# Optimization experiments

Measured on AMD Instinct MI355X. Metric: run time of the kernel, lower is better.

The kernel has to match this reference:

```python
import jax, jax.numpy as jnp
import numpy as np
from jax import lax

SHIFT_SIZE = 5
PAD = SHIFT_SIZE // 2


def _chunk_shifts(C):
    # torch.chunk(x, 5, dim=1): chunk size = ceil(C/5); shift for chunk i is i - PAD
    csz = -(-C // SHIFT_SIZE)
    return jnp.arange(C) // csz - PAD  # (C,) in [-PAD, PAD]


def _shift_along_h(x, shifts):
    # x: (B,C,H,W). Equivalent of pad+chunk+roll(dim=2)+cat+narrow: per-channel
    # zero-filled shift along H (no wraparound since |shift| <= PAD).
    B, C, H, W = x.shape
    xp = jnp.pad(x, ((0, 0), (0, 0), (PAD, PAD), (0, 0)))
    c_idx = jnp.arange(C)[:, None]              # (C,1)
    h_idx = jnp.arange(H)[None, :] + PAD - shifts[:, None]  # (C,H)
    return xp[:, c_idx, h_idx, :]               # (B,C,H,W)


def _shift_along_w(x, shifts):
    return jnp.swapaxes(_shift_along_h(jnp.swapaxes(x, 2, 3), shifts), 2, 3)


def setup_inputs() -> dict:
    key = jax.random.key(0)
    ks = jax.random.split(key, 7)
    B, H, W, C, hidden = 8, 128, 128, 256, 256
    x = jax.random.normal(ks[0], (B, H * W, C), dtype=jnp.float32)
    w1 = jax.random.normal(ks[1], (hidden, C), dtype=jnp.float32) * 0.02
    b1 = jnp.zeros((hidden,), dtype=jnp.float32)
    fan_out = 3 * 3 * hidden // hidden  # groups = hidden
    dw_w = jax.random.normal(ks[2], (hidden, 1, 3, 3), dtype=jnp.float32) * np.sqrt(2.0 / fan_out)
    dw_b = jnp.zeros((hidden,), dtype=jnp.float32)
    w2 = jax.random.normal(ks[3], (C, hidden), dtype=jnp.float32) * 0.02
    b2 = jnp.zeros((C,), dtype=jnp.float32)
    return {"x": x, "H": H, "W": W, "w1": w1, "b1": b1,
            "dw_w": dw_w, "dw_b": dw_b, "w2": w2, "b2": b2}


def reference(x, H, W, w1, b1, dw_w, dw_b, w2, b2):
    B, N, C = x.shape
    shifts = _chunk_shifts(C)

    # --- shift along H, then fc1 ---
    xn = jnp.reshape(jnp.swapaxes(x, 1, 2), (B, C, H, W))
    x_s = _shift_along_h(xn, shifts)
    x_s = jnp.swapaxes(x_s.reshape(B, C, H * W), 1, 2)   # (B,N,C)
    h = x_s @ w1.T + b1                                  # (B,N,hidden)

    # --- depthwise 3x3 conv ---
    Ch = h.shape[-1]
    himg = jnp.reshape(jnp.swapaxes(h, 1, 2), (B, Ch, H, W))
    himg = lax.conv_general_dilated(
        himg, dw_w, window_strides=(1, 1), padding=((1, 1), (1, 1)),
        feature_group_count=Ch,
        dimension_numbers=("NCHW", "OIHW", "NCHW")) + dw_b[None, :, None, None]
    h = jnp.swapaxes(himg.reshape(B, Ch, H * W), 1, 2)

    h = jax.nn.gelu(h, approximate=False)

    # --- shift along W, then fc2 ---
    hn = jnp.reshape(jnp.swapaxes(h, 1, 2), (B, Ch, H, W))
    h_s = _shift_along_w(hn, _chunk_shifts(Ch))
    h_s = jnp.swapaxes(h_s.reshape(B, Ch, H * W), 1, 2)  # (B,N,hidden)
    out = h_s @ w2.T + b2                                # (B,N,C)
    return out
```

## Files before the change

kernel.cpp:

```cpp
#include <hip/hip_runtime.h>
#include <hip/hip_bf16.h>
#include <math.h>

#define Hc   128
#define Wc   128
#define Cc   256
#define Nc   (Hc * Wc)
#define Bn   8
#define Mtot (Bn * Nc)
#define CSZ  52
#define SPAD 2

typedef unsigned short ushort4v __attribute__((ext_vector_type(4)));
typedef unsigned short ushort8  __attribute__((ext_vector_type(8)));
typedef __bf16         bf16x8   __attribute__((ext_vector_type(8)));
typedef float          f32x4    __attribute__((ext_vector_type(4)));

__device__ __forceinline__ float bf2f(unsigned short u) {
    return __uint_as_float(((unsigned)u) << 16);
}
__device__ __forceinline__ unsigned short f2bf(float f) {
    unsigned u = __float_as_uint(f);
    return (unsigned short)((u + 0x7fffu + ((u >> 16) & 1u)) >> 16);
}
__device__ __forceinline__ unsigned pk2bf(float a, float b) {
    unsigned ua = __float_as_uint(a) + 0x8000u;
    unsigned ub = __float_as_uint(b) + 0x8000u;
    return __builtin_amdgcn_perm(ub, ua, 0x07060302);
}
__device__ __forceinline__ void async16(const void* g, void* l) {
    __builtin_amdgcn_global_load_lds(
        (const __attribute__((address_space(1))) unsigned*)g,
        (__attribute__((address_space(3))) unsigned*)l, 16, 0, 0);
}

__global__ __launch_bounds__(256)
void wprep_kernel(const float* __restrict__ w1, const float* __restrict__ dw_w,
                  unsigned short* __restrict__ w1b, float* __restrict__ dwT)
{
    const int g = blockIdx.x * 256 + threadIdx.x;
    {
        float4 a = *(const float4*)(w1 + (size_t)g * 4);
        ushort4v o = { f2bf(a.x), f2bf(a.y), f2bf(a.z), f2bf(a.w) };
        *(ushort4v*)(w1b + (size_t)g * 4) = o;
    }
    if (g < 9 * Cc) dwT[(g % 9) * Cc + g / 9] = dw_w[g];
}

__global__ __launch_bounds__(256)
void fc1_mfma_kernel(const float* __restrict__ x, const unsigned short* __restrict__ w1b,
                     const float* __restrict__ b1, unsigned short* __restrict__ h1)
{
    __shared__ __bf16 As[128 * 32];
    __shared__ __bf16 Bs[128 * 32];
    __shared__ __align__(16) unsigned short Cs[128 * 136];

    const int tid  = threadIdx.x;
    const int lane = tid & 63;
    const int wave = tid >> 6;
    const int wm = (wave >> 1) * 64, wn = (wave & 1) * 64;
    const int bx = blockIdx.x;
    const size_t m0 = (size_t)bx * 128;
    const int j0 = blockIdx.y * 128;
    const int bb = bx >> 7, hh = bx & 127;
    const int r = tid >> 1, half = tid & 1;
    const int idx0 = tid, idx1 = tid + 256;

    f32x4 acc[4][4] = {};
    for (int k0 = 0; k0 < Cc; k0 += 32) {
        async16(w1b + (size_t)(j0 + (idx0 >> 2)) * Cc + k0 + (idx0 & 3) * 8, Bs + idx0 * 8);
        async16(w1b + (size_t)(j0 + (idx1 >> 2)) * Cc + k0 + (idx1 & 3) * 8, Bs + idx1 * 8);
        {
            const int kb = k0 + half * 16;
            unsigned p[8];
#pragma unroll
            for (int j = 0; j < 4; ++j) {
                const int c  = kb + j * 4;
                const int s  = c / CSZ - SPAD;
                const int hs = hh - s;
                float4 v = make_float4(0.f, 0.f, 0.f, 0.f);
                if (hs >= 0 && hs < Hc)
                    v = *(const float4*)(x + ((size_t)(bb * Nc + hs * Wc + r)) * Cc + c);
                p[j * 2]     = pk2bf(v.x, v.y);
                p[j * 2 + 1] = pk2bf(v.z, v.w);
            }
            uint4 q0, q1;
            q0.x = p[0]; q0.y = p[1]; q0.z = p[2]; q0.w = p[3];
            q1.x = p[4]; q1.y = p[5]; q1.z = p[6]; q1.w = p[7];
            *(uint4*)(As + r * 32 + half * 16)     = q0;
            *(uint4*)(As + r * 32 + half * 16 + 8) = q1;
        }
        __syncthreads();
        bf16x8 a[4], b[4];
        const int kq = (lane >> 4) * 8;
        const int rr = lane & 15;
#pragma unroll
        for (int i = 0; i < 4; ++i) {
            a[i] = *(const bf16x8*)(As + (wm + i * 16 + rr) * 32 + kq);
            b[i] = *(const bf16x8*)(Bs + (wn + i * 16 + rr) * 32 + kq);
        }
#pragma unroll
        for (int i = 0; i < 4; ++i)
#pragma unroll
            for (int j = 0; j < 4; ++j)
                acc[i][j] = __builtin_amdgcn_mfma_f32_16x16x32_bf16(a[i], b[j], acc[i][j], 0, 0, 0);
        __syncthreads();
    }

    const int cq = (lane >> 4) * 4;
    const int cc = lane & 15;
    float bv[4];
#pragma unroll
    for (int j = 0; j < 4; ++j) bv[j] = b1[j0 + wn + j * 16 + cc];
#pragma unroll
    for (int i = 0; i < 4; ++i)
#pragma unroll
        for (int j = 0; j < 4; ++j) {
            const int col = wn + j * 16 + cc;
#pragma unroll
            for (int rg = 0; rg < 4; ++rg)
                Cs[(wm + i * 16 + cq + rg) * 136 + col] = f2bf(acc[i][j][rg] + bv[j]);
        }
    __syncthreads();
    {
        const int row = tid >> 1, hf = tid & 1;
        const unsigned short* src = Cs + row * 136 + hf * 64;
        unsigned short* dst = h1 + (m0 + row) * Cc + j0 + hf * 64;
#pragma unroll
        for (int i = 0; i < 8; ++i)
            *(uint4*)(dst + i * 8) = *(const uint4*)(src + i * 8);
    }
}

__global__ __launch_bounds__(256)
void zero_borders_kernel(unsigned short* __restrict__ gsh)
{
    const int gid = blockIdx.x * 256 + threadIdx.x;
    const int cg  = gid & 31;
    const int rest = gid >> 5;
    const int wi = rest & 3;
    const int bh = rest >> 2;
    const int w  = (wi & 2) ? (wi + 124) : wi;
    uint4 z; z.x = z.y = z.z = z.w = 0u;
    *(uint4*)(gsh + ((size_t)bh * 128 + w) * Cc + cg * 8) = z;
}

__global__ __launch_bounds__(256)
void dwconv_gelu_scatter_kernel(const unsigned short* __restrict__ h1,
                                const float* __restrict__ dwT, const float* __restrict__ dw_b,
                                unsigned short* __restrict__ gsh)
{
    const int t   = threadIdx.x;
    const int cg  = t & 31;
    const int wq  = t >> 5;
    const int c0  = cg * 8;
    const int bh  = blockIdx.x >> 2;
    const int qtr = blockIdx.x & 3;
    const int bb  = bh >> 7, hh = bh & 127;
    const size_t rowb = (size_t)bb * Nc + (size_t)hh * Wc;
    const int wbase = qtr * 32 + wq * 4 - 1;

    float acc[4][8];
    {
        float4 a0 = *(const float4*)(dw_b + c0);
        float4 a1 = *(const float4*)(dw_b + c0 + 4);
#pragma unroll
        for (int i = 0; i < 4; ++i) {
            acc[i][0] = a0.x; acc[i][1] = a0.y; acc[i][2] = a0.z; acc[i][3] = a0.w;
            acc[i][4] = a1.x; acc[i][5] = a1.y; acc[i][6] = a1.z; acc[i][7] = a1.w;
        }
    }

#pragma unroll
    for (int dy = -1; dy <= 1; ++dy) {
        const int y = hh + dy;
        if (y < 0 || y >= Hc) continue;
        const unsigned short* rp = h1 + ((size_t)bb * Nc + (size_t)y * Wc) * Cc + c0;
        float in[6][8];
#pragma unroll
        for (int dx = 0; dx < 6; ++dx) {
            const int w = wbase + dx;
            ushort8 raw = {0, 0, 0, 0, 0, 0, 0, 0};
            if (w >= 0 && w < Wc) raw = *(const ushort8*)(rp + (size_t)w * Cc);
#pragma unroll
            for (int c = 0; c < 8; ++c) in[dx][c] = bf2f(raw[c]);
        }
        const float* wrow = dwT + (dy + 1) * 3 * Cc + c0;
        float wr[3][8];
#pragma unroll
        for (int tx = 0; tx < 3; ++tx) {
            float4 wa = *(const float4*)(wrow + tx * Cc);
            float4 wb = *(const float4*)(wrow + tx * Cc + 4);
            wr[tx][0] = wa.x; wr[tx][1] = wa.y; wr[tx][2] = wa.z; wr[tx][3] = wa.w;
            wr[tx][4] = wb.x; wr[tx][5] = wb.y; wr[tx][6] = wb.z; wr[tx][7] = wb.w;
        }
#pragma unroll
        for (int i = 0; i < 4; ++i)
#pragma unroll
            for (int tx = 0; tx < 3; ++tx)
#pragma unroll
                for (int c = 0; c < 8; ++c)
                    acc[i][c] += in[i + tx][c] * wr[tx][c];
    }

    const int s0 = c0 / CSZ - SPAD;
    const int s1 = (c0 + 4) / CSZ - SPAD;
#pragma unroll
    for (int i = 0; i < 4; ++i) {
        float g[8];
#pragma unroll
        for (int c = 0; c < 8; ++c) {
            const float v = acc[i][c];
            const float u = v * v;
            const float a = __builtin_fmaf(0.0713548162f, u, 1.5957691216f);
            const float e = __expf(v * a);
            g[c] = v * e * __builtin_amdgcn_rcpf(e + 1.0f);
        }
        uint2 lo, hi;
        lo.x = pk2bf(g[0], g[1]); lo.y = pk2bf(g[2], g[3]);
        hi.x = pk2bf(g[4], g[5]); hi.y = pk2bf(g[6], g[7]);
        const int wo = wbase + 1 + i;
        const int w0 = wo + s0, w1 = wo + s1;
        if ((unsigned)w0 < (unsigned)Wc) *(uint2*)(gsh + (rowb + w0) * Cc + c0)     = lo;
        if ((unsigned)w1 < (unsigned)Wc) *(uint2*)(gsh + (rowb + w1) * Cc + c0 + 4) = hi;
    }
}

__global__ __launch_bounds__(256)
void fc2_mfma_kernel(const unsigned short* __restrict__ A, const float* __restrict__ w2,
                     const float* __restrict__ b2, float* __restrict__ out)
{
    __shared__ __bf16 As[128 * 32];
    __shared__ __bf16 Bs[128 * 32];

    const int tid  = threadIdx.x;
    const int lane = tid & 63;
    const int wave = tid >> 6;
    const int wm = (wave >> 1) * 64, wn = (wave & 1) * 64;
    const size_t m0 = (size_t)blockIdx.x * 128;
    const int j0 = blockIdx.y * 128;

    const int idx0 = tid, idx1 = tid + 256;
    const int brow = tid >> 1, bch = (tid & 1) * 16;

    f32x4 acc[4][4] = {};
    for (int k0 = 0; k0 < Cc; k0 += 32) {
        async16(A + (m0 + (idx0 >> 2)) * Cc + k0 + (idx0 & 3) * 8, As + idx0 * 8);
        async16(A + (m0 + (idx1 >> 2)) * Cc + k0 + (idx1 & 3) * 8, As + idx1 * 8);
        {
            const float* src = w2 + (size_t)(j0 + brow) * Cc + k0 + bch;
            float4 v0 = *(const float4*)(src);
            float4 v1 = *(const float4*)(src + 4);
            float4 v2 = *(const float4*)(src + 8);
            float4 v3 = *(const float4*)(src + 12);
            uint4 p0, p1;
            p0.x = pk2bf(v0.x, v0.y); p0.y = pk2bf(v0.z, v0.w);
            p0.z = pk2bf(v1.x, v1.y); p0.w = pk2bf(v1.z, v1.w);
            p1.x = pk2bf(v2.x, v2.y); p1.y = pk2bf(v2.z, v2.w);
            p1.z = pk2bf(v3.x, v3.y); p1.w = pk2bf(v3.z, v3.w);
            *(uint4*)(Bs + brow * 32 + bch)     = p0;
            *(uint4*)(Bs + brow * 32 + bch + 8) = p1;
        }
        __syncthreads();
        bf16x8 a[4], b[4];
        const int kq = (lane >> 4) * 8;
        const int rr = lane & 15;
#pragma unroll
        for (int i = 0; i < 4; ++i) {
            a[i] = *(const bf16x8*)(As + (wm + i * 16 + rr) * 32 + kq);
            b[i] = *(const bf16x8*)(Bs + (wn + i * 16 + rr) * 32 + kq);
        }
#pragma unroll
        for (int i = 0; i < 4; ++i)
#pragma unroll
            for (int j = 0; j < 4; ++j)
                acc[i][j] = __builtin_amdgcn_mfma_f32_16x16x32_bf16(a[i], b[j], acc[i][j], 0, 0, 0);
        __syncthreads();
    }

    const int cq = (lane >> 4) * 4;
    const int cc = lane & 15;
    float bv[4];
#pragma unroll
    for (int j = 0; j < 4; ++j) bv[j] = b2[j0 + wn + j * 16 + cc];
#pragma unroll
    for (int i = 0; i < 4; ++i)
#pragma unroll
        for (int j = 0; j < 4; ++j) {
            const int col = j0 + wn + j * 16 + cc;
#pragma unroll
            for (int rg = 0; rg < 4; ++rg)
                out[(m0 + wm + i * 16 + cq + rg) * Cc + col] = acc[i][j][rg] + bv[j];
        }
}

extern "C" void kernel_launch(void* const* d_in, const int* in_sizes, int n_in,
                              void* d_out, int out_size, void* d_ws, size_t ws_size,
                              hipStream_t stream) {
    const float* x    = (const float*)d_in[0];
    const float* w1   = (const float*)d_in[3];
    const float* b1   = (const float*)d_in[4];
    const float* dw_w = (const float*)d_in[5];
    const float* dw_b = (const float*)d_in[6];
    const float* w2   = (const float*)d_in[7];
    const float* b2   = (const float*)d_in[8];
    float* out = (float*)d_out;

    unsigned short* h1  = (unsigned short*)d_ws;
    unsigned short* gsh = h1 + (size_t)Mtot * Cc;
    unsigned short* w1b = (unsigned short*)d_out;
    float*          dwT = (float*)(w1b + 65536);

    wprep_kernel<<<dim3(64), dim3(256), 0, stream>>>(w1, dw_w, w1b, dwT);
    fc1_mfma_kernel<<<dim3(Mtot / 128, 2), dim3(256), 0, stream>>>(x, w1b, b1, h1);
    zero_borders_kernel<<<dim3(512), dim3(256), 0, stream>>>(gsh);
    dwconv_gelu_scatter_kernel<<<dim3(4 * Mtot / 128), dim3(256), 0, stream>>>(h1, dwT, dw_b, gsh);
    fc2_mfma_kernel<<<dim3(Mtot / 128, 2), dim3(256), 0, stream>>>(gsh, w2, b2, out);
}
```

Baseline: 387.8 us.

## Double-buffer fc1/fc2 GEMM K-loop with padded LDS and XCD-aware block remap

Both GEMM kernels now use double-buffered LDS tiles. The next K-slice's global loads (register-staged for fp32 operands, async for bf16) are issued before the current MFMA block, so load latency overlaps compute. The register-converted operand tile is padded to a 40-element stride to reduce LDS bank conflicts, and fc1 reuses one shared buffer for the epilogue tile. The 2D grid is flattened to 1D with a block-index swizzle across 8 XCDs, plus a launch_bounds occupancy hint, at the cost of more registers for the in-flight loads.

```diff
diff --git a/kernel.cpp b/kernel.cpp
--- a/kernel.cpp
+++ b/kernel.cpp
@@ -47,64 +47,90 @@
     if (g < 9 * Cc) dwT[(g % 9) * Cc + g / 9] = dw_w[g];
 }
 
-__global__ __launch_bounds__(256)
+__global__ __launch_bounds__(256, 4)
 void fc1_mfma_kernel(const float* __restrict__ x, const unsigned short* __restrict__ w1b,
                      const float* __restrict__ b1, unsigned short* __restrict__ h1)
 {
-    __shared__ __bf16 As[128 * 32];
-    __shared__ __bf16 Bs[128 * 32];
-    __shared__ __align__(16) unsigned short Cs[128 * 136];
+    __shared__ __align__(16) unsigned char smem[36864];
+    __bf16* As = (__bf16*)smem;
+    __bf16* Bs = (__bf16*)(smem + 20480);
+    unsigned short* Cs = (unsigned short*)smem;
 
     const int tid  = threadIdx.x;
     const int lane = tid & 63;
     const int wave = tid >> 6;
     const int wm = (wave >> 1) * 64, wn = (wave & 1) * 64;
-    const int bx = blockIdx.x;
+
+    const int lid = ((blockIdx.x & 7) << 8) | (blockIdx.x >> 3);
+    const int bx  = lid >> 1;
+    const int j0  = (lid & 1) * 128;
     const size_t m0 = (size_t)bx * 128;
-    const int j0 = blockIdx.y * 128;
     const int bb = bx >> 7, hh = bx & 127;
     const int r = tid >> 1, half = tid & 1;
     const int idx0 = tid, idx1 = tid + 256;
 
+    float4 av[4];
+    auto loadA = [&](int t) {
+        const int kb = t * 32 + half * 16;
+#pragma unroll
+        for (int j = 0; j < 4; ++j) {
+            const int c  = kb + j * 4;
+            const int s  = c / CSZ - SPAD;
+            const int hs = hh - s;
+            av[j] = make_float4(0.f, 0.f, 0.f, 0.f);
+            if (hs >= 0 && hs < Hc)
+                av[j] = *(const float4*)(x + ((size_t)(bb * Nc + hs * Wc + r)) * Cc + c);
+        }
+    };
+    auto storeA = [&](int buf) {
+        uint4 q0, q1;
+        q0.x = pk2bf(av[0].x, av[0].y); q0.y = pk2bf(av[0].z, av[0].w);
+        q0.z = pk2bf(av[1].x, av[1].y); q0.w = pk2bf(av[1].z, av[1].w);
+        q1.x = pk2bf(av[2].x, av[2].y); q1.y = pk2bf(av[2].z, av[2].w);
+        q1.z = pk2bf(av[3].x, av[3].y); q1.w = pk2bf(av[3].z, av[3].w);
+        __bf16* dst = As + buf * (128 * 40) + r * 40 + half * 16;
+        *(uint4*)dst       = q0;
+        *(uint4*)(dst + 8) = q1;
+    };
+    auto stageB = [&](int buf, int t) {
+        const int k0 = t * 32;
+        __bf16* bdst = Bs + buf * (128 * 32);
+        async16(w1b + (size_t)(j0 + (idx0 >> 2)) * Cc + k0 + (idx0 & 3) * 8, bdst + idx0 * 8);
+        async16(w1b + (size_t)(j0 + (idx1 >> 2)) * Cc + k0 + (idx1 & 3) * 8, bdst + idx1 * 8);
+    };
+
     f32x4 acc[4][4] = {};
-    for (int k0 = 0; k0 < Cc; k0 += 32) {
-        async16(w1b + (size_t)(j0 + (idx0 >> 2)) * Cc + k0 + (idx0 & 3) * 8, Bs + idx0 * 8);
-        async16(w1b + (size_t)(j0 + (idx1 >> 2)) * Cc + k0 + (idx1 & 3) * 8, Bs + idx1 * 8);
-        {
-            const int kb = k0 + half * 16;
-            unsigned p[8];
-#pragma unroll
-            for (int j = 0; j < 4; ++j) {
-                const int c  = kb + j * 4;
-                const int s  = c / CSZ - SPAD;
-                const int hs = hh - s;
-                float4 v = make_float4(0.f, 0.f, 0.f, 0.f);
-                if (hs >= 0 && hs < Hc)
-                    v = *(const float4*)(x + ((size_t)(bb * Nc + hs * Wc + r)) * Cc + c);
-                p[j * 2]     = pk2bf(v.x, v.y);
-                p[j * 2 + 1] = pk2bf(v.z, v.w);
-            }
-            uint4 q0, q1;
-            q0.x = p[0]; q0.y = p[1]; q0.z = p[2]; q0.w = p[3];
-            q1.x = p[4]; q1.y = p[5]; q1.z = p[6]; q1.w = p[7];
-            *(uint4*)(As + r * 32 + half * 16)     = q0;
-            *(uint4*)(As + r * 32 + half * 16 + 8) = q1;
-        }
-        __syncthreads();
+
+    loadA(0);
+    stageB(0, 0);
+    storeA(0);
+    __syncthreads();
+
+    const int kq = (lane >> 4) * 8;
+    const int rr = lane & 15;
+    int cur = 0;
+    for (int t = 0; t < 8; ++t) {
+        const int nxt = cur ^ 1;
+        if (t < 7) {
+            loadA(t + 1);
+            stageB(nxt, t + 1);
+        }
         bf16x8 a[4], b[4];
-        const int kq = (lane >> 4) * 8;
-        const int rr = lane & 15;
+        const __bf16* ap = As + cur * (128 * 40);
+        const __bf16* bp = Bs + cur * (128 * 32);
 #pragma unroll
         for (int i = 0; i < 4; ++i) {
-            a[i] = *(const bf16x8*)(As + (wm + i * 16 + rr) * 32 + kq);
-            b[i] = *(const bf16x8*)(Bs + (wn + i * 16 + rr) * 32 + kq);
+            a[i] = *(const bf16x8*)(ap + (wm + i * 16 + rr) * 40 + kq);
+            b[i] = *(const bf16x8*)(bp + (wn + i * 16 + rr) * 32 + kq);
         }
 #pragma unroll
         for (int i = 0; i < 4; ++i)
 #pragma unroll
             for (int j = 0; j < 4; ++j)
                 acc[i][j] = __builtin_amdgcn_mfma_f32_16x16x32_bf16(a[i], b[j], acc[i][j], 0, 0, 0);
+        if (t < 7) storeA(nxt);
         __syncthreads();
+        cur = nxt;
     }
 
     const int cq = (lane >> 4) * 4;
@@ -226,56 +252,83 @@
     }
 }
 
-__global__ __launch_bounds__(256)
+__global__ __launch_bounds__(256, 4)
 void fc2_mfma_kernel(const unsigned short* __restrict__ A, const float* __restrict__ w2,
                      const float* __restrict__ b2, float* __restrict__ out)
 {
-    __shared__ __bf16 As[128 * 32];
-    __shared__ __bf16 Bs[128 * 32];
+    __shared__ __align__(16) unsigned char smem[36864];
+    __bf16* As = (__bf16*)smem;
+    __bf16* Bs = (__bf16*)(smem + 16384);
 
     const int tid  = threadIdx.x;
     const int lane = tid & 63;
     const int wave = tid >> 6;
     const int wm = (wave >> 1) * 64, wn = (wave & 1) * 64;
-    const size_t m0 = (size_t)blockIdx.x * 128;
-    const int j0 = blockIdx.y * 128;
+
+    const int lid = ((blockIdx.x & 7) << 8) | (blockIdx.x >> 3);
+    const size_t m0 = (size_t)(lid >> 1) * 128;
+    const int j0 = (lid & 1) * 128;
 
     const int idx0 = tid, idx1 = tid + 256;
     const int brow = tid >> 1, bch = (tid & 1) * 16;
 
+    float4 wv[4];
+    auto loadB = [&](int t) {
+        const float* src = w2 + (size_t)(j0 + brow) * Cc + t * 32 + bch;
+        wv[0] = *(const float4*)(src);
+        wv[1] = *(const float4*)(src + 4);
+        wv[2] = *(const float4*)(src + 8);
+        wv[3] = *(const float4*)(src + 12);
+    };
+    auto storeB = [&](int buf) {
+        uint4 p0, p1;
+        p0.x = pk2bf(wv[0].x, wv[0].y); p0.y = pk2bf(wv[0].z, wv[0].w);
+        p0.z = pk2bf(wv[1].x, wv[1].y); p0.w = pk2bf(wv[1].z, wv[1].w);
+        p1.x = pk2bf(wv[2].x, wv[2].y); p1.y = pk2bf(wv[2].z, wv[2].w);
+        p1.z = pk2bf(wv[3].x, wv[3].y); p1.w = pk2bf(wv[3].z, wv[3].w);
+        __bf16* dst = Bs + buf * (128 * 40) + brow * 40 + bch;
+        *(uint4*)dst       = p0;
+        *(uint4*)(dst + 8) = p1;
+    };
+    auto stageA = [&](int buf, int t) {
+        const int k0 = t * 32;
+        __bf16* adst = As + buf * (128 * 32);
+        async16(A + (m0 + (idx0 >> 2)) * Cc + k0 + (idx0 & 3) * 8, adst + idx0 * 8);
+        async16(A + (m0 + (idx1 >> 2)) * Cc + k0 + (idx1 & 3) * 8, adst + idx1 * 8);
+    };
+
     f32x4 acc[4][4] = {};
-    for (int k0 = 0; k0 < Cc; k0 += 32) {
-        async16(A + (m0 + (idx0 >> 2)) * Cc + k0 + (idx0 & 3) * 8, As + idx0 * 8);
-        async16(A + (m0 + (idx1 >> 2)) * Cc + k0 + (idx1 & 3) * 8, As + idx1 * 8);
-        {
-            const float* src = w2 + (size_t)(j0 + brow) * Cc + k0 + bch;
-            float4 v0 = *(const float4*)(src);
-            float4 v1 = *(const float4*)(src + 4);
-            float4 v2 = *(const float4*)(src + 8);
-            float4 v3 = *(const float4*)(src + 12);
-            uint4 p0, p1;
-            p0.x = pk2bf(v0.x, v0.y); p0.y = pk2bf(v0.z, v0.w);
-            p0.z = pk2bf(v1.x, v1.y); p0.w = pk2bf(v1.z, v1.w);
-            p1.x = pk2bf(v2.x, v2.y); p1.y = pk2bf(v2.z, v2.w);
-            p1.z = pk2bf(v3.x, v3.y); p1.w = pk2bf(v3.z, v3.w);
-            *(uint4*)(Bs + brow * 32 + bch)     = p0;
-            *(uint4*)(Bs + brow * 32 + bch + 8) = p1;
-        }
-        __syncthreads();
+
+    loadB(0);
+    stageA(0, 0);
+    storeB(0);
+    __syncthreads();
+
+    const int kq = (lane >> 4) * 8;
+    const int rr = lane & 15;
+    int cur = 0;
+    for (int t = 0; t < 8; ++t) {
+        const int nxt = cur ^ 1;
+        if (t < 7) {
+            loadB(t + 1);
+            stageA(nxt, t + 1);
+        }
         bf16x8 a[4], b[4];
-        const int kq = (lane >> 4) * 8;
-        const int rr = lane & 15;
+        const __bf16* ap = As + cur * (128 * 32);
+        const __bf16* bp = Bs + cur * (128 * 40);
 #pragma unroll
         for (int i = 0; i < 4; ++i) {
-            a[i] = *(const bf16x8*)(As + (wm + i * 16 + rr) * 32 + kq);
-            b[i] = *(const bf16x8*)(Bs + (wn + i * 16 + rr) * 32 + kq);
+            a[i] = *(const bf16x8*)(ap + (wm + i * 16 + rr) * 32 + kq);
+            b[i] = *(const bf16x8*)(bp + (wn + i * 16 + rr) * 40 + kq);
         }
 #pragma unroll
         for (int i = 0; i < 4; ++i)
 #pragma unroll
             for (int j = 0; j < 4; ++j)
                 acc[i][j] = __builtin_amdgcn_mfma_f32_16x16x32_bf16(a[i], b[j], acc[i][j], 0, 0, 0);
+        if (t < 7) storeB(nxt);
         __syncthreads();
+        cur = nxt;
     }
 
     const int cq = (lane >> 4) * 4;
@@ -312,8 +365,8 @@
     float*          dwT = (float*)(w1b + 65536);
 
     wprep_kernel<<<dim3(64), dim3(256), 0, stream>>>(w1, dw_w, w1b, dwT);
-    fc1_mfma_kernel<<<dim3(Mtot / 128, 2), dim3(256), 0, stream>>>(x, w1b, b1, h1);
+    fc1_mfma_kernel<<<dim3(2 * Mtot / 128), dim3(256), 0, stream>>>(x, w1b, b1, h1);
     zero_borders_kernel<<<dim3(512), dim3(256), 0, stream>>>(gsh);
     dwconv_gelu_scatter_kernel<<<dim3(4 * Mtot / 128), dim3(256), 0, stream>>>(h1, dwT, dw_b, gsh);
-    fc2_mfma_kernel<<<dim3(Mtot / 128, 2), dim3(256), 0, stream>>>(gsh, w2, b2, out);
-}
+    fc2_mfma_kernel<<<dim3(2 * Mtot / 128), dim3(256), 0, stream>>>(gsh, w2, b2, out);
+}
```

Result: slower. 414.4 us (+6.8%).
